# Optimization experiments

Hardware: AMD Instinct MI355X
Metric: run time of the kernel (lower is better)

The kernel has to match this reference:

```python
import jax, jax.numpy as jnp
import numpy as np

G, K, R = 33, 8, 8
B, HL, WL, HF, WF = 4, 256, 256, 1080, 1920


def setup_inputs() -> dict:
    key = jax.random.key(0)
    ks = jax.random.split(key, 14)

    def n(k, shape, std=0.05):
        return jax.random.normal(k, shape, jnp.float32) * std

    # identity LUT [G,G,G,3] + small noise per basis, clamped to [0,1]
    rg = jnp.linspace(0.0, 1.0, G)
    Rr, Gg, Bb = jnp.meshgrid(rg, rg, rg, indexing='ij')
    ident = jnp.stack([Rr, Gg, Bb], axis=-1)
    bases = jnp.clip(ident[None] + jax.random.normal(ks[0], (K, G, G, G, 3), jnp.float32) * 0.01, 0.0, 1.0)

    return {
        'img_lr': jax.random.uniform(ks[1], (B, 3, HL, WL), jnp.float32),
        'img_full': jax.random.uniform(ks[2], (B, 3, HF, WF), jnp.float32),
        'bases': bases,
        'wp_c1_w': n(ks[3], (16, 3, 3, 3)), 'wp_c1_b': jnp.zeros(16, jnp.float32),
        'wp_c2_w': n(ks[4], (32, 16, 3, 3)), 'wp_c2_b': jnp.zeros(32, jnp.float32),
        'wp_fc_w': n(ks[5], (K, 32)), 'wp_fc_b': jnp.ones(K, jnp.float32),  # bias init 1.0
        'rp_c1_w': n(ks[6], (16, 3, 3, 3)), 'rp_c1_b': jnp.zeros(16, jnp.float32),
        'rp_c2_w': n(ks[7], (32, 16, 3, 3)), 'rp_c2_b': jnp.zeros(32, jnp.float32),
        'rp_fcu_w': n(ks[8], (R * G, 32)), 'rp_fcu_b': jnp.zeros(R * G, jnp.float32),
        'rp_fcv_w': n(ks[9], (R * G, 32)), 'rp_fcv_b': jnp.zeros(R * G, jnp.float32),
        'rp_fcw_w': n(ks[10], (R * G, 32)), 'rp_fcw_b': jnp.zeros(R * G, jnp.float32),
        'rp_fcc_w': n(ks[11], (R * 3, 32), std=0.1), 'rp_fcc_b': jnp.zeros(R * 3, jnp.float32),  # std=0.1, zero bias
    }


def _conv(x, w, b):
    y = jax.lax.conv_general_dilated(x, w, (2, 2), ((1, 1), (1, 1)),
                                     dimension_numbers=('NCHW', 'OIHW', 'NCHW'))
    return y + b[None, :, None, None]


def _encode(x, c1w, c1b, c2w, c2b):
    h = jax.nn.relu(_conv(x, c1w, c1b))
    h = jax.nn.relu(_conv(h, c2w, c2b))
    return h.mean((2, 3))  # AdaptiveAvgPool2d(1) -> [B,32]


def _trilinear(img, lut):
    # img: [B,3,H,W] in [0,1]; lut: [B,G,G,G,3]
    b, _, h, w = img.shape
    g = lut.shape[1]
    xyz = jnp.clip(jnp.transpose(img, (0, 2, 3, 1)) * (g - 1), 0.0, g - 1 - 1e-6)  # [B,H,W,3]
    i0 = jnp.floor(xyz).astype(jnp.int32)
    x0, y0, z0 = i0[..., 0], i0[..., 1], i0[..., 2]
    x1 = jnp.minimum(x0 + 1, g - 1)
    y1 = jnp.minimum(y0 + 1, g - 1)
    z1 = jnp.minimum(z0 + 1, g - 1)
    d = xyz - i0.astype(xyz.dtype)
    xd, yd, zd = d[..., 0:1], d[..., 1:2], d[..., 2:3]  # [B,H,W,1]
    lut_flat = lut.reshape(b, g * g * g, 3)

    def gather(ix, iy, iz):
        idx = ((ix * g + iy) * g + iz).reshape(b, -1, 1)
        return jnp.take_along_axis(lut_flat, idx, axis=1).reshape(b, h, w, 3)

    c000 = gather(x0, y0, z0); c100 = gather(x1, y0, z0)
    c010 = gather(x0, y1, z0); c110 = gather(x1, y1, z0)
    c001 = gather(x0, y0, z1); c101 = gather(x1, y0, z1)
    c011 = gather(x0, y1, z1); c111 = gather(x1, y1, z1)
    c00 = c000 * (1 - xd) + c100 * xd
    c01 = c001 * (1 - xd) + c101 * xd
    c10 = c010 * (1 - xd) + c110 * xd
    c11 = c011 * (1 - xd) + c111 * xd
    c0 = c00 * (1 - yd) + c10 * yd
    c1 = c01 * (1 - yd) + c11 * yd
    out = c0 * (1 - zd) + c1 * zd
    return jnp.transpose(out, (0, 3, 1, 2))  # [B,3,H,W]


def reference(img_lr, img_full, bases,
              wp_c1_w, wp_c1_b, wp_c2_w, wp_c2_b, wp_fc_w, wp_fc_b,
              rp_c1_w, rp_c1_b, rp_c2_w, rp_c2_b,
              rp_fcu_w, rp_fcu_b, rp_fcv_w, rp_fcv_b,
              rp_fcw_w, rp_fcw_b, rp_fcc_w, rp_fcc_b):
    b = img_lr.shape[0]
    # WeightPredictor: raw unnormalized alpha [B,K]
    alpha = _encode(img_lr, wp_c1_w, wp_c1_b, wp_c2_w, wp_c2_b) @ wp_fc_w.T + wp_fc_b
    # ResidualPredictor (note: no softmax/tanh applied in the source forward)
    hr = _encode(img_lr, rp_c1_w, rp_c1_b, rp_c2_w, rp_c2_b)
    u = (hr @ rp_fcu_w.T + rp_fcu_b).reshape(b, R, G)
    v = (hr @ rp_fcv_w.T + rp_fcv_b).reshape(b, R, G)
    w_ = (hr @ rp_fcw_w.T + rp_fcw_b).reshape(b, R, G)
    c = (hr @ rp_fcc_w.T + rp_fcc_b).reshape(b, R, 3)
    # CP residual -> [B,G,G,G,3]
    delta = jnp.einsum('brx,bry,brz,brc->bxyzc', u, v, w_, c)
    # fuse bases with raw alpha and add residual
    L = jnp.einsum('bk,kxyzc->bxyzc', alpha, bases) + delta
    out = _trilinear(img_full, L)
    delta_norm = jnp.mean(jnp.abs(delta))
    return (out, alpha, delta, L, delta_norm)
```

## Files before the change

kernel.cpp:

```cpp
#include <hip/hip_runtime.h>
#include <stdint.h>

#define GN   33
#define GG   1089
#define GGG  35937
#define BATCH 4
#define HFULL 1080
#define WFULL 1920
#define NPIX (HFULL*WFULL)
#define NPIX4 (NPIX/4)

#define OUT_ALPHA 24883200
#define OUT_DELTA 24883232
#define OUT_L     25314476
#define OUT_DNORM 25745720

#define WS_LUT64B 0
#define WS_PART   2300000
#define WS_DN     2308192
#define NLUTBLK   132

typedef float  float4n __attribute__((ext_vector_type(4)));
typedef unsigned int uint4n __attribute__((ext_vector_type(4)));

__device__ __forceinline__ unsigned short f2bf(float f) {
    unsigned u = __float_as_uint(f);
    unsigned r = (u + 0x7fffu + ((u >> 16) & 1u)) >> 16;
    return (unsigned short)r;
}
__device__ __forceinline__ float bflo(unsigned u) { return __uint_as_float(u << 16); }
__device__ __forceinline__ float bfhi(unsigned u) { return __uint_as_float(u & 0xffff0000u); }

__global__ __launch_bounds__(256) void encoder_kernel(
    const float* __restrict__ img,
    const float* __restrict__ w1wp, const float* __restrict__ b1wp,
    const float* __restrict__ w2wp, const float* __restrict__ b2wp,
    const float* __restrict__ w1rp, const float* __restrict__ b1rp,
    const float* __restrict__ w2rp, const float* __restrict__ b2rp,
    float* __restrict__ ws)
{
    const int bi = blockIdx.x;
    const int enc = bi >> 7, b = (bi >> 5) & 3, rt = (bi >> 1) & 15, ct = bi & 1;
    const float* w1 = enc ? w1rp : w1wp;
    const float* b1 = enc ? b1rp : b1wp;
    const float* w2 = enc ? w2rp : w2wp;
    const float* b2 = enc ? b2rp : b2wp;
    __shared__ float simg[3][19][132];
    __shared__ float sh1[4][9][66];
    __shared__ float red[4][16];
    const float* imb = img + (size_t)b * 3 * 65536;
    const int tid = threadIdx.x;

    for (int l = tid; l < 3 * 19 * 131; l += 256) {
        const int c = l / (19 * 131);
        const int rem = l - c * (19 * 131);
        const int rw = rem / 131, cl = rem - rw * 131;
        const int gr = 16 * rt - 3 + rw, gc = 128 * ct - 3 + cl;
        float v = 0.f;
        if ((unsigned)gr < 256u && (unsigned)gc < 256u)
            v = imb[(c << 16) + (gr << 8) + gc];
        simg[c][rw][cl] = v;
    }
    __syncthreads();

    const int p = tid & 127, h = tid >> 7;
    const int prow = p >> 5, pcol = p & 31;
    float acc[16];
    #pragma unroll
    for (int o = 0; o < 16; ++o) acc[o] = b2[h * 16 + o];

    for (int cc0 = 0; cc0 < 16; cc0 += 4) {
        if (cc0) __syncthreads();
        for (int l = tid; l < 4 * 9 * 65; l += 256) {
            const int oc = l / (9 * 65);
            const int rem = l - oc * (9 * 65);
            const int r = rem / 65, cl = rem - r * 65;
            const int hrow = 8 * rt - 1 + r, hcol = 64 * ct - 1 + cl;
            float v = 0.f;
            if ((unsigned)hrow < 128u && (unsigned)hcol < 128u) {
                float a1 = b1[cc0 + oc];
                const float* wo = w1 + (cc0 + oc) * 27;
                #pragma unroll
                for (int c = 0; c < 3; ++c)
                    #pragma unroll
                    for (int ky = 0; ky < 3; ++ky)
                        #pragma unroll
                        for (int kx = 0; kx < 3; ++kx)
                            a1 += wo[c * 9 + ky * 3 + kx] * simg[c][2 * r + ky][2 * cl + kx];
                v = fmaxf(a1, 0.f);
            }
            sh1[oc][r][cl] = v;
        }
        __syncthreads();
        #pragma unroll
        for (int cc = 0; cc < 4; ++cc) {
            float vv[9];
            #pragma unroll
            for (int ky = 0; ky < 3; ++ky)
                #pragma unroll
                for (int kx = 0; kx < 3; ++kx)
                    vv[ky * 3 + kx] = sh1[cc][2 * prow + ky][2 * pcol + kx];
            #pragma unroll
            for (int o = 0; o < 16; ++o) {
                const float* wo = w2 + (h * 16 + o) * 144 + (cc0 + cc) * 9;
                #pragma unroll
                for (int k = 0; k < 9; ++k) acc[o] += wo[k] * vv[k];
            }
        }
    }
    const int lane = tid & 63, wv = tid >> 6;
    #pragma unroll
    for (int o = 0; o < 16; ++o) {
        float v = fmaxf(acc[o], 0.f);
        #pragma unroll
        for (int off = 32; off; off >>= 1) v += __shfl_down(v, off);
        if (lane == 0) red[wv][o] = v;
    }
    __syncthreads();
    if (tid < 32) {
        const int o = tid & 15, g = tid >> 4;
        const float s = red[g * 2][o] + red[g * 2 + 1][o];
        ws[WS_PART + ((enc * 4 + b) * 32 + (rt * 2 + ct)) * 32 + g * 16 + o] = s;
    }
}

__global__ __launch_bounds__(256) void lut_kernel(
    const float* __restrict__ bases,
    const float* __restrict__ wp_fc_w, const float* __restrict__ wp_fc_b,
    const float* __restrict__ fcu_w, const float* __restrict__ fcu_b,
    const float* __restrict__ fcv_w, const float* __restrict__ fcv_b,
    const float* __restrict__ fcw_w, const float* __restrict__ fcw_b,
    const float* __restrict__ fcc_w, const float* __restrict__ fcc_b,
    float* __restrict__ ws, float* __restrict__ dout)
{
    const int b = blockIdx.x & 3;
    const int x = blockIdx.x >> 2;
    const int x1 = min(x + 1, GN - 1);
    const int tid = threadIdx.x;
    __shared__ float mean[2][32];
    __shared__ float U[264], V[264], W[264], Cc[24], Al[8];
    __shared__ float Lp[2][GG * 3];

    if (tid < 64) {
        const int enc = tid >> 5, o = tid & 31;
        const float* pp = ws + WS_PART + (enc * 4 + b) * 1024 + o;
        float s = 0.f;
        #pragma unroll
        for (int i = 0; i < 32; ++i) s += pp[i * 32];
        mean[enc][o] = s * (1.f / 4096.f);
    }
    __syncthreads();
    for (int r = tid; r < 824; r += 256) {
        if (r < 8) {
            const float* row = wp_fc_w + r * 32;
            float a = wp_fc_b[r];
            #pragma unroll 8
            for (int q = 0; q < 32; ++q) a += row[q] * mean[0][q];
            Al[r] = a;
            dout[OUT_ALPHA + b * 8 + r] = a;
        } else if (r < 272) {
            const int jj = r - 8;
            const float* row = fcu_w + jj * 32;
            float a = fcu_b[jj];
            #pragma unroll 8
            for (int q = 0; q < 32; ++q) a += row[q] * mean[1][q];
            U[jj] = a;
        } else if (r < 536) {
            const int jj = r - 272;
            const float* row = fcv_w + jj * 32;
            float a = fcv_b[jj];
            #pragma unroll 8
            for (int q = 0; q < 32; ++q) a += row[q] * mean[1][q];
            V[jj] = a;
        } else if (r < 800) {
            const int jj = r - 536;
            const float* row = fcw_w + jj * 32;
            float a = fcw_b[jj];
            #pragma unroll 8
            for (int q = 0; q < 32; ++q) a += row[q] * mean[1][q];
            W[jj] = a;
        } else {
            const int jj = r - 800;
            const float* row = fcc_w + jj * 32;
            float a = fcc_b[jj];
            #pragma unroll 8
            for (int q = 0; q < 32; ++q) a += row[q] * mean[1][q];
            Cc[jj] = a;
        }
    }
    __syncthreads();

    float ux0[8], ux1[8], cr[8][3];
    #pragma unroll
    for (int r = 0; r < 8; ++r) {
        ux0[r] = U[r * GN + x];
        ux1[r] = U[r * GN + x1];
        cr[r][0] = Cc[r * 3 + 0];
        cr[r][1] = Cc[r * 3 + 1];
        cr[r][2] = Cc[r * 3 + 2];
    }

    float sum3 = 0.f;
    #pragma unroll
    for (int px = 0; px < 2; ++px) {
        const int xi = px ? x1 : x;
        for (int i = tid; i < GG; i += 256) {
            const int y = i / GN, z = i - y * GN;
            float d0 = 0.f, d1 = 0.f, d2 = 0.f;
            #pragma unroll
            for (int r = 0; r < 8; ++r) {
                const float t = (px ? ux1[r] : ux0[r]) * V[r * GN + y] * W[r * GN + z];
                d0 += t * cr[r][0];
                d1 += t * cr[r][1];
                d2 += t * cr[r][2];
            }
            float l0 = d0, l1 = d1, l2 = d2;
            const float* bp = bases + (size_t)(xi * GG + i) * 3;
            #pragma unroll
            for (int k = 0; k < 8; ++k) {
                const float a = Al[k];
                const float* bk = bp + (size_t)k * GGG * 3;
                l0 += a * bk[0];
                l1 += a * bk[1];
                l2 += a * bk[2];
            }
            Lp[px][i * 3 + 0] = l0;
            Lp[px][i * 3 + 1] = l1;
            Lp[px][i * 3 + 2] = l2;
            if (px == 0) {
                const size_t o3 = ((size_t)b * GGG + x * GG + i) * 3;
                dout[OUT_DELTA + o3 + 0] = d0;
                dout[OUT_DELTA + o3 + 1] = d1;
                dout[OUT_DELTA + o3 + 2] = d2;
                dout[OUT_L + o3 + 0] = l0;
                dout[OUT_L + o3 + 1] = l1;
                dout[OUT_L + o3 + 2] = l2;
                sum3 += fabsf(d0) + fabsf(d1) + fabsf(d2);
            }
        }
    }
    __syncthreads();

    for (int i = tid; i < GG; i += 256) {
        const int y = i / GN, z = i - y * GN;
        const int y1 = min(y + 1, GN - 1), z1 = min(z + 1, GN - 1);
        const int i00 = (y  * GN + z ) * 3, i01 = (y  * GN + z1) * 3;
        const int i10 = (y1 * GN + z ) * 3, i11 = (y1 * GN + z1) * 3;
        uint4 wr, wg, wb;
        #pragma unroll
        for (int c = 0; c < 3; ++c) {
            const unsigned w00 = (unsigned)f2bf(Lp[0][i00 + c]) | ((unsigned)f2bf(Lp[0][i01 + c]) << 16);
            const unsigned w01 = (unsigned)f2bf(Lp[0][i10 + c]) | ((unsigned)f2bf(Lp[0][i11 + c]) << 16);
            const unsigned w10 = (unsigned)f2bf(Lp[1][i00 + c]) | ((unsigned)f2bf(Lp[1][i01 + c]) << 16);
            const unsigned w11 = (unsigned)f2bf(Lp[1][i10 + c]) | ((unsigned)f2bf(Lp[1][i11 + c]) << 16);
            uint4& wv = c == 0 ? wr : (c == 1 ? wg : wb);
            wv.x = w00; wv.y = w01; wv.z = w10; wv.w = w11;
        }
        uint4* dst = (uint4*)((char*)ws + WS_LUT64B) + ((size_t)b * GGG + x * GG + i) * 4;
        dst[0] = wr; dst[1] = wg; dst[2] = wb;
    }

    #pragma unroll
    for (int off = 32; off; off >>= 1) sum3 += __shfl_down(sum3, off);
    __shared__ float s4[4];
    const int lane = tid & 63, wid = tid >> 6;
    if (!lane) s4[wid] = sum3;
    __syncthreads();
    if (!tid) ws[WS_DN + blockIdx.x] = s4[0] + s4[1] + s4[2] + s4[3];
}

__global__ __launch_bounds__(256) void apply_kernel(
    const float* __restrict__ img,
    const float* __restrict__ ws, float* __restrict__ dout)
{
    if (blockIdx.x == 0 && threadIdx.x < 64) {
        float s = 0.f;
        for (int i = threadIdx.x; i < NLUTBLK; i += 64) s += ws[WS_DN + i];
        #pragma unroll
        for (int off = 32; off; off >>= 1) s += __shfl_down(s, off);
        if (threadIdx.x == 0)
            dout[OUT_DNORM] = s * (1.0f / (float)(BATCH * GGG * 3));
    }
    const int b = blockIdx.x & 3;
    const int q = (blockIdx.x >> 2) * 256 + threadIdx.x;
    const float4n* base = (const float4n*)(img + (size_t)b * 3 * NPIX);
    const float4n rv = __builtin_nontemporal_load(&base[q]);
    const float4n gv = __builtin_nontemporal_load(&base[NPIX4 + q]);
    const float4n bv = __builtin_nontemporal_load(&base[2 * NPIX4 + q]);
    const uint4* lut = (const uint4*)((const char*)ws + WS_LUT64B) + (size_t)b * GGG * 4;

    float rrr[4] = {rv.x, rv.y, rv.z, rv.w};
    float ggg[4] = {gv.x, gv.y, gv.z, gv.w};
    float bbb[4] = {bv.x, bv.y, bv.z, bv.w};
    int idx[4]; float xd[4], yd[4], zd[4];
    #pragma unroll
    for (int t = 0; t < 4; ++t) {
        const float xf = fminf(fmaxf(rrr[t] * 32.f, 0.f), 31.999998f);
        const float yf = fminf(fmaxf(ggg[t] * 32.f, 0.f), 31.999998f);
        const float zf = fminf(fmaxf(bbb[t] * 32.f, 0.f), 31.999998f);
        const int x0 = (int)xf, y0 = (int)yf, z0 = (int)zf;
        xd[t] = xf - (float)x0; yd[t] = yf - (float)y0; zd[t] = zf - (float)z0;
        idx[t] = (x0 * GN + y0) * GN + z0;
    }
    uint4 er[4], eg[4], eb[4];
    #pragma unroll
    for (int t = 0; t < 4; ++t) {
        const uint4* e = lut + (size_t)idx[t] * 4;
        er[t] = e[0]; eg[t] = e[1]; eb[t] = e[2];
    }
    float o0[4], o1[4], o2[4];
    #pragma unroll
    for (int t = 0; t < 4; ++t) {
        {
            const float z00 = bflo(er[t].x) + zd[t] * (bfhi(er[t].x) - bflo(er[t].x));
            const float z01 = bflo(er[t].y) + zd[t] * (bfhi(er[t].y) - bflo(er[t].y));
            const float z10 = bflo(er[t].z) + zd[t] * (bfhi(er[t].z) - bflo(er[t].z));
            const float z11 = bflo(er[t].w) + zd[t] * (bfhi(er[t].w) - bflo(er[t].w));
            const float y0v = z00 + yd[t] * (z01 - z00);
            const float y1v = z10 + yd[t] * (z11 - z10);
            o0[t] = y0v + xd[t] * (y1v - y0v);
        }
        {
            const float z00 = bflo(eg[t].x) + zd[t] * (bfhi(eg[t].x) - bflo(eg[t].x));
            const float z01 = bflo(eg[t].y) + zd[t] * (bfhi(eg[t].y) - bflo(eg[t].y));
            const float z10 = bflo(eg[t].z) + zd[t] * (bfhi(eg[t].z) - bflo(eg[t].z));
            const float z11 = bflo(eg[t].w) + zd[t] * (bfhi(eg[t].w) - bflo(eg[t].w));
            const float y0v = z00 + yd[t] * (z01 - z00);
            const float y1v = z10 + yd[t] * (z11 - z10);
            o1[t] = y0v + xd[t] * (y1v - y0v);
        }
        {
            const float z00 = bflo(eb[t].x) + zd[t] * (bfhi(eb[t].x) - bflo(eb[t].x));
            const float z01 = bflo(eb[t].y) + zd[t] * (bfhi(eb[t].y) - bflo(eb[t].y));
            const float z10 = bflo(eb[t].z) + zd[t] * (bfhi(eb[t].z) - bflo(eb[t].z));
            const float z11 = bflo(eb[t].w) + zd[t] * (bfhi(eb[t].w) - bflo(eb[t].w));
            const float y0v = z00 + yd[t] * (z01 - z00);
            const float y1v = z10 + yd[t] * (z11 - z10);
            o2[t] = y0v + xd[t] * (y1v - y0v);
        }
    }
    float4n* ob = (float4n*)(dout + (size_t)b * 3 * NPIX);
    float4n s0; s0.x = o0[0]; s0.y = o0[1]; s0.z = o0[2]; s0.w = o0[3];
    float4n s1; s1.x = o1[0]; s1.y = o1[1]; s1.z = o1[2]; s1.w = o1[3];
    float4n s2; s2.x = o2[0]; s2.y = o2[1]; s2.z = o2[2]; s2.w = o2[3];
    __builtin_nontemporal_store(s0, &ob[q]);
    __builtin_nontemporal_store(s1, &ob[NPIX4 + q]);
    __builtin_nontemporal_store(s2, &ob[2 * NPIX4 + q]);
}

extern "C" void kernel_launch(void* const* d_in, const int* in_sizes, int n_in,
                              void* d_out, int out_size, void* d_ws, size_t ws_size,
                              hipStream_t stream)
{
    const float* img_lr   = (const float*)d_in[0];
    const float* img_full = (const float*)d_in[1];
    const float* bases    = (const float*)d_in[2];
    const float* wp_c1_w  = (const float*)d_in[3];
    const float* wp_c1_b  = (const float*)d_in[4];
    const float* wp_c2_w  = (const float*)d_in[5];
    const float* wp_c2_b  = (const float*)d_in[6];
    const float* wp_fc_w  = (const float*)d_in[7];
    const float* wp_fc_b  = (const float*)d_in[8];
    const float* rp_c1_w  = (const float*)d_in[9];
    const float* rp_c1_b  = (const float*)d_in[10];
    const float* rp_c2_w  = (const float*)d_in[11];
    const float* rp_c2_b  = (const float*)d_in[12];
    const float* fcu_w    = (const float*)d_in[13];
    const float* fcu_b    = (const float*)d_in[14];
    const float* fcv_w    = (const float*)d_in[15];
    const float* fcv_b    = (const float*)d_in[16];
    const float* fcw_w    = (const float*)d_in[17];
    const float* fcw_b    = (const float*)d_in[18];
    const float* fcc_w    = (const float*)d_in[19];
    const float* fcc_b    = (const float*)d_in[20];
    float* ws  = (float*)d_ws;
    float* out = (float*)d_out;

    encoder_kernel<<<dim3(256), 256, 0, stream>>>(
        img_lr, wp_c1_w, wp_c1_b, wp_c2_w, wp_c2_b,
        rp_c1_w, rp_c1_b, rp_c2_w, rp_c2_b, ws);
    lut_kernel<<<dim3(NLUTBLK), 256, 0, stream>>>(
        bases, wp_fc_w, wp_fc_b, fcu_w, fcu_b, fcv_w, fcv_b,
        fcw_w, fcw_b, fcc_w, fcc_b, ws, out);
    apply_kernel<<<dim3(BATCH * NPIX4 / 256), 256, 0, stream>>>(img_full, ws, out);
}
```

Measured before the change: 362.1 us.

## Cooperatively gather LUT cells across four lanes and transpose outputs through LDS

The apply kernel now splits each pixel's 64-byte packed LUT cell across a quad of lanes. Each lane loads one 16-byte channel chunk for pixels whose coordinates it receives from its neighbours via shuffles. Results are staged in padded shared memory and transposed back, so each thread still writes its own float4 outputs. The aim is to replace three separate 16-byte scattered loads per pixel with one contiguous 64-byte access per quad. The cost is a wasted fourth lane per cell, extra shuffles, an LDS round trip with a barrier, and a launch-bounds occupancy hint.

```diff
diff --git a/kernel.cpp b/kernel.cpp
--- a/kernel.cpp
+++ b/kernel.cpp
@@ -269,10 +269,12 @@
     if (!tid) ws[WS_DN + blockIdx.x] = s4[0] + s4[1] + s4[2] + s4[3];
 }
 
-__global__ __launch_bounds__(256) void apply_kernel(
+__global__ __launch_bounds__(256, 4) void apply_kernel(
     const float* __restrict__ img,
     const float* __restrict__ ws, float* __restrict__ dout)
 {
+    __shared__ float so[3 * 1093];
+
     if (blockIdx.x == 0 && threadIdx.x < 64) {
         float s = 0.f;
         for (int i = threadIdx.x; i < NLUTBLK; i += 64) s += ws[WS_DN + i];
@@ -282,7 +284,8 @@
             dout[OUT_DNORM] = s * (1.0f / (float)(BATCH * GGG * 3));
     }
     const int b = blockIdx.x & 3;
-    const int q = (blockIdx.x >> 2) * 256 + threadIdx.x;
+    const int tid = threadIdx.x;
+    const int q = (blockIdx.x >> 2) * 256 + tid;
     const float4n* base = (const float4n*)(img + (size_t)b * 3 * NPIX);
     const float4n rv = __builtin_nontemporal_load(&base[q]);
     const float4n gv = __builtin_nontemporal_load(&base[NPIX4 + q]);
@@ -302,47 +305,36 @@
         xd[t] = xf - (float)x0; yd[t] = yf - (float)y0; zd[t] = zf - (float)z0;
         idx[t] = (x0 * GN + y0) * GN + z0;
     }
-    uint4 er[4], eg[4], eb[4];
-    #pragma unroll
-    for (int t = 0; t < 4; ++t) {
-        const uint4* e = lut + (size_t)idx[t] * 4;
-        er[t] = e[0]; eg[t] = e[1]; eb[t] = e[2];
-    }
-    float o0[4], o1[4], o2[4];
-    #pragma unroll
-    for (int t = 0; t < 4; ++t) {
-        {
-            const float z00 = bflo(er[t].x) + zd[t] * (bfhi(er[t].x) - bflo(er[t].x));
-            const float z01 = bflo(er[t].y) + zd[t] * (bfhi(er[t].y) - bflo(er[t].y));
-            const float z10 = bflo(er[t].z) + zd[t] * (bfhi(er[t].z) - bflo(er[t].z));
-            const float z11 = bflo(er[t].w) + zd[t] * (bfhi(er[t].w) - bflo(er[t].w));
-            const float y0v = z00 + yd[t] * (z01 - z00);
-            const float y1v = z10 + yd[t] * (z11 - z10);
-            o0[t] = y0v + xd[t] * (y1v - y0v);
-        }
-        {
-            const float z00 = bflo(eg[t].x) + zd[t] * (bfhi(eg[t].x) - bflo(eg[t].x));
-            const float z01 = bflo(eg[t].y) + zd[t] * (bfhi(eg[t].y) - bflo(eg[t].y));
-            const float z10 = bflo(eg[t].z) + zd[t] * (bfhi(eg[t].z) - bflo(eg[t].z));
-            const float z11 = bflo(eg[t].w) + zd[t] * (bfhi(eg[t].w) - bflo(eg[t].w));
-            const float y0v = z00 + yd[t] * (z01 - z00);
-            const float y1v = z10 + yd[t] * (z11 - z10);
-            o1[t] = y0v + xd[t] * (y1v - y0v);
-        }
-        {
-            const float z00 = bflo(eb[t].x) + zd[t] * (bfhi(eb[t].x) - bflo(eb[t].x));
-            const float z01 = bflo(eb[t].y) + zd[t] * (bfhi(eb[t].y) - bflo(eb[t].y));
-            const float z10 = bflo(eb[t].z) + zd[t] * (bfhi(eb[t].z) - bflo(eb[t].z));
-            const float z11 = bflo(eb[t].w) + zd[t] * (bfhi(eb[t].w) - bflo(eb[t].w));
-            const float y0v = z00 + yd[t] * (z01 - z00);
-            const float y1v = z10 + yd[t] * (z11 - z10);
-            o2[t] = y0v + xd[t] * (y1v - y0v);
-        }
-    }
+
+    const int sub = tid & 3;
+    const int qd  = tid >> 2;
+    #pragma unroll
+    for (int r = 0; r < 16; ++r) {
+        const int src = r >> 2, sl = r & 3;
+        const int   pidx = __shfl(idx[sl], src, 4);
+        const float pxd  = __shfl(xd[sl],  src, 4);
+        const float pyd  = __shfl(yd[sl],  src, 4);
+        const float pzd  = __shfl(zd[sl],  src, 4);
+        const uint4 e = lut[(size_t)(unsigned)pidx * 4 + sub];
+        const float e0l = bflo(e.x), e1l = bflo(e.y), e2l = bflo(e.z), e3l = bflo(e.w);
+        const float z00 = e0l + pzd * (bfhi(e.x) - e0l);
+        const float z01 = e1l + pzd * (bfhi(e.y) - e1l);
+        const float z10 = e2l + pzd * (bfhi(e.z) - e2l);
+        const float z11 = e3l + pzd * (bfhi(e.w) - e3l);
+        const float y0v = z00 + pyd * (z01 - z00);
+        const float y1v = z10 + pyd * (z11 - z10);
+        const float ov  = y0v + pxd * (y1v - y0v);
+        if (sub < 3) so[sub * 1093 + qd * 17 + r] = ov;
+    }
+    __syncthreads();
+
+    const int pb = 4 * tid + qd;
+    float4n s0, s1, s2;
+    s0.x = so[pb + 0];        s0.y = so[pb + 1];        s0.z = so[pb + 2];        s0.w = so[pb + 3];
+    s1.x = so[1093 + pb + 0]; s1.y = so[1093 + pb + 1]; s1.z = so[1093 + pb + 2]; s1.w = so[1093 + pb + 3];
+    s2.x = so[2186 + pb + 0]; s2.y = so[2186 + pb + 1]; s2.z = so[2186 + pb + 2]; s2.w = so[2186 + pb + 3];
+
     float4n* ob = (float4n*)(dout + (size_t)b * 3 * NPIX);
-    float4n s0; s0.x = o0[0]; s0.y = o0[1]; s0.z = o0[2]; s0.w = o0[3];
-    float4n s1; s1.x = o1[0]; s1.y = o1[1]; s1.z = o1[2]; s1.w = o1[3];
-    float4n s2; s2.x = o2[0]; s2.y = o2[1]; s2.z = o2[2]; s2.w = o2[3];
     __builtin_nontemporal_store(s0, &ob[q]);
     __builtin_nontemporal_store(s1, &ob[NPIX4 + q]);
     __builtin_nontemporal_store(s2, &ob[2 * NPIX4 + q]);
```

Result: faster. 309.7 us (-14.5%).
